# Performance work log

Measured on AMD Instinct MI355X. Metric: run time of the kernel, lower is better.

The kernel has to match this reference:

```python
import jax, jax.numpy as jnp
import numpy as np

B, T, I, H, O = 256, 1024, 128, 256, 64


def setup_inputs() -> dict:
    key = jax.random.key(0)
    ks = jax.random.split(key, 8)
    s_ih = 1.0 / np.sqrt(H)
    return {
        "x": jax.random.normal(ks[0], (B, T, I), dtype=jnp.float32),
        "W_ih": jax.random.normal(ks[1], (3 * H, I), dtype=jnp.float32) * s_ih,
        "W_hh": jax.random.normal(ks[2], (3 * H, H), dtype=jnp.float32) * s_ih,
        "b_ih": jax.random.normal(ks[3], (3 * H,), dtype=jnp.float32) * s_ih,
        "b_hh": jax.random.normal(ks[4], (3 * H,), dtype=jnp.float32) * s_ih,
        "alpha": jax.random.normal(ks[5], (H,), dtype=jnp.float32),
        "fc_w": jax.random.normal(ks[6], (O, H), dtype=jnp.float32) * s_ih,
        "fc_b": jax.random.normal(ks[7], (O,), dtype=jnp.float32) * s_ih,
    }


def _pagru_last_hidden(x, W_ih, W_hh, b_ih, b_hh, alpha):
    # Precompute all input-side gate projections in one big GEMM: [T, B, 3H]
    xg = jnp.einsum("bti,gi->tbg", x, W_ih) + b_ih
    a = jax.nn.sigmoid(alpha)  # per-unit adaptive interpolation gate

    def step(h, gi):
        gh = h @ W_hh.T + b_hh                      # [B, 3H]
        i_r, i_z, i_n = jnp.split(gi, 3, axis=-1)
        h_r, h_z, h_n = jnp.split(gh, 3, axis=-1)
        r = jax.nn.sigmoid(i_r + h_r)
        z = jax.nn.sigmoid(i_z + h_z)
        n = jnp.tanh(i_n + r * h_n)
        h_new = (1.0 - z) * n + z * h               # torch GRUCell convention
        h_out = a * h_new + (1.0 - a) * h           # parameter-adaptive update
        return h_out, None

    h0 = jnp.zeros((x.shape[0], W_hh.shape[1]), dtype=x.dtype)
    h_last, _ = jax.lax.scan(step, h0, xg)
    return h_last


def reference(x, W_ih, W_hh, b_ih, b_hh, alpha, fc_w, fc_b):
    h_last = _pagru_last_hidden(x, W_ih, W_hh, b_ih, b_hh, alpha)
    return jax.nn.sigmoid(h_last @ fc_w.T + fc_b)   # [B, O]
```

## Files before the change

kernel.cpp:

```cpp
#include <hip/hip_runtime.h>
#include <cstdint>
#include <cstddef>

#define TT 1024
#define BB 256
#define II 128
#define HH 256
#define GG 768
#define OO 64
#define TCH 256
#define NCH (TT / TCH)

typedef float f32x4 __attribute__((ext_vector_type(4)));
typedef short short8 __attribute__((ext_vector_type(8)));

__device__ __forceinline__ unsigned f2bf(float f) {
  unsigned u = __builtin_bit_cast(unsigned, f);
  return (u + 0x7FFFu + ((u >> 16) & 1u)) >> 16;
}
__device__ __forceinline__ float bflo(unsigned p) {
  return __builtin_bit_cast(float, p << 16);
}
__device__ __forceinline__ float bfhi(unsigned p) {
  return __builtin_bit_cast(float, p & 0xffff0000u);
}
__device__ __forceinline__ unsigned cvtpk_bf16(float lo, float hi) {
  unsigned r;
  asm("v_cvt_pk_bf16_f32 %0, %1, %2" : "=v"(r) : "v"(lo), "v"(hi));
  return r;
}
__device__ __forceinline__ float sigm(float x) {
  return __builtin_amdgcn_rcpf(1.f + __builtin_amdgcn_exp2f(-1.44269504088896f * x));
}

__global__ void k_btot(const float* __restrict__ bih, const float* __restrict__ bhh,
                       float* __restrict__ btot) {
  int i = blockIdx.x * 256 + threadIdx.x;
  if (i < GG) btot[i] = bih[i] + (i < 512 ? bhh[i] : 0.f);
}

__global__ __attribute__((amdgpu_flat_work_group_size(512, 512), amdgpu_waves_per_eu(2, 2)))
void k_xg(const float* __restrict__ x,
    const float* __restrict__ Wih, const float* __restrict__ btot,
    unsigned short* __restrict__ xg, int t0)
{
  __shared__ unsigned short xlds[BB * II];
  const int tid = threadIdx.x;
  const int tl = blockIdx.x;
  const int tg = t0 + tl;
  const int w = tid >> 6, lane = tid & 63, cu = lane & 15, quad = lane >> 4;

  for (int i = 0; i < 16; ++i) {
    int cid = tid + i * 512;
    int row = cid >> 5, c16 = cid & 31;
    const float4 v = *(const float4*)(x + (size_t)row * TT * II + (size_t)tg * II + c16 * 4);
    unsigned lo = f2bf(v.x) | (f2bf(v.y) << 16);
    unsigned hi = f2bf(v.z) | (f2bf(v.w) << 16);
    int byt = (row * 256 + c16 * 8) ^ ((row & 7) << 4);
    *(uint2*)((char*)xlds + byt) = make_uint2(lo, hi);
  }

  uint4 WA[3][2][4];
  float bias[3][2][4];
  #pragma unroll
  for (int pp = 0; pp < 3; ++pp)
    #pragma unroll
    for (int t2 = 0; t2 < 2; ++t2) {
      int ut = w * 6 + pp * 2 + t2;
      int grow = ut * 16 + cu;
      const float4* wr = (const float4*)(Wih + (size_t)grow * II);
      #pragma unroll
      for (int kk = 0; kk < 4; ++kk) {
        float4 lo = wr[kk * 8 + quad * 2];
        float4 hi = wr[kk * 8 + quad * 2 + 1];
        uint4 pk;
        pk.x = f2bf(lo.x) | (f2bf(lo.y) << 16);
        pk.y = f2bf(lo.z) | (f2bf(lo.w) << 16);
        pk.z = f2bf(hi.x) | (f2bf(hi.y) << 16);
        pk.w = f2bf(hi.z) | (f2bf(hi.w) << 16);
        WA[pp][t2][kk] = pk;
      }
      #pragma unroll
      for (int j = 0; j < 4; ++j)
        bias[pp][t2][j] = btot[ut * 16 + quad * 4 + j];
    }
  __syncthreads();

  #pragma unroll 1
  for (int mt = 0; mt < 16; ++mt) {
    short8 bf[4];
    int brow = mt * 16 + cu;
    #pragma unroll
    for (int kk = 0; kk < 4; ++kk) {
      int byt = (brow * 256 + kk * 64 + quad * 16) ^ ((cu & 7) << 4);
      bf[kk] = *(const short8*)((const char*)xlds + byt);
    }
    f32x4 acc[3][2];
    #pragma unroll
    for (int pp = 0; pp < 3; ++pp) {
      acc[pp][0] = (f32x4){0.f, 0.f, 0.f, 0.f};
      acc[pp][1] = (f32x4){0.f, 0.f, 0.f, 0.f};
    }
    #pragma unroll
    for (int kk = 0; kk < 4; ++kk)
      #pragma unroll
      for (int pp = 0; pp < 3; ++pp)
        #pragma unroll
        for (int t2 = 0; t2 < 2; ++t2)
          acc[pp][t2] = __builtin_amdgcn_mfma_f32_16x16x32_bf16(
              __builtin_bit_cast(short8, WA[pp][t2][kk]), bf[kk], acc[pp][t2], 0, 0, 0);
    #pragma unroll
    for (int pp = 0; pp < 3; ++pp)
      #pragma unroll
      for (int t2 = 0; t2 < 2; ++t2) {
        int ut = w * 6 + pp * 2 + t2;
        unsigned p0 = cvtpk_bf16(acc[pp][t2][0] + bias[pp][t2][0],
                                 acc[pp][t2][1] + bias[pp][t2][1]);
        unsigned p1 = cvtpk_bf16(acc[pp][t2][2] + bias[pp][t2][2],
                                 acc[pp][t2][3] + bias[pp][t2][3]);
        size_t rec = ((size_t)(tl * 16 + mt) * 48 + ut) * 64 + lane;
        ((uint2*)xg)[rec] = make_uint2(p0, p1);
      }
  }
}

__global__ __launch_bounds__(1024, 4) void k_scan(const float* __restrict__ Whh,
    const float* __restrict__ bhh, const float* __restrict__ alpha,
    const unsigned short* __restrict__ xg, float* __restrict__ hlast, int t0)
{
  __shared__ unsigned short hbuf[2][16384];
  __shared__ uint4 wlds[16][3][64];
  const int tid = threadIdx.x, wv = tid >> 6, lane = tid & 63;
  const int cu = lane & 15, quad = lane >> 4;
  const int wg = blockIdx.x;

  uint4 Wf[3][7];
  #pragma unroll
  for (int g = 0; g < 3; ++g) {
    int grow = g * 256 + wv * 16 + cu;
    const float4* wr = (const float4*)(Whh + (size_t)grow * HH);
    #pragma unroll
    for (int kk = 0; kk < 8; ++kk) {
      float4 lo = wr[kk * 8 + quad * 2];
      float4 hi = wr[kk * 8 + quad * 2 + 1];
      uint4 pk;
      pk.x = cvtpk_bf16(lo.x, lo.y);
      pk.y = cvtpk_bf16(lo.z, lo.w);
      pk.z = cvtpk_bf16(hi.x, hi.y);
      pk.w = cvtpk_bf16(hi.z, hi.w);
      if (kk < 7) Wf[g][kk] = pk;
      else        wlds[wv][g][lane] = pk;
    }
  }
  const int u0 = wv * 16 + quad * 4;
  unsigned asigp[2], bhp[2];
  asigp[0] = cvtpk_bf16(sigm(alpha[u0]),     sigm(alpha[u0 + 1]));
  asigp[1] = cvtpk_bf16(sigm(alpha[u0 + 2]), sigm(alpha[u0 + 3]));
  bhp[0] = f2bf(bhh[512 + u0])     | (f2bf(bhh[512 + u0 + 1]) << 16);
  bhp[1] = f2bf(bhh[512 + u0 + 2]) | (f2bf(bhh[512 + u0 + 3]) << 16);

  for (int i = 0; i < 4; ++i) {
    int idx = tid * 4 + i;
    int m = idx >> 8, u = idx & 255;
    float hv = (t0 == 0) ? 0.f : hlast[((size_t)wg * 16 + m) * 256 + u];
    int byt = (m * 512 + u * 2) ^ ((m & 7) << 4) ^ ((m >> 3) << 6);
    *(unsigned short*)((char*)hbuf[0] + byt) = (unsigned short)f2bf(hv);
  }
  __syncthreads();

  const unsigned swz = (unsigned)(((cu & 7) << 4) ^ ((cu >> 3) << 6));
  const unsigned vb  = (unsigned)((cu * 512 + quad * 16)) ^ swz;
  const unsigned whp = (unsigned)((cu * 512 + wv * 32 + quad * 8)) ^ swz;

  const uint2* xq = (const uint2*)xg + ((size_t)wg * 48 + wv) * 64 + lane;
  uint2 qn0 = xq[0], qn1 = xq[1024], qn2 = xq[2048];

  unsigned bufb = 0;
  const char* hbase = (const char*)hbuf;

  for (int tl = 0; tl < TCH; ++tl) {
    const char* hs = hbase + bufb;
    f32x4 acc[3];
    acc[0][0]=bflo(qn0.x); acc[0][1]=bfhi(qn0.x); acc[0][2]=bflo(qn0.y); acc[0][3]=bfhi(qn0.y);
    acc[1][0]=bflo(qn1.x); acc[1][1]=bfhi(qn1.x); acc[1][2]=bflo(qn1.y); acc[1][3]=bfhi(qn1.y);
    acc[2][0]=bflo(bhp[0]); acc[2][1]=bfhi(bhp[0]);
    acc[2][2]=bflo(bhp[1]); acc[2][3]=bfhi(bhp[1]);
    uint2 q2c = qn2;
    if (tl < TCH - 1) xq += 49152;
    qn0 = xq[0]; qn1 = xq[1024]; qn2 = xq[2048];
    uint2 hpq = *(const uint2*)(hs + whp);

    #pragma unroll
    for (int kk = 0; kk < 7; ++kk) {
      short8 bfh = *(const short8*)(hs + (vb ^ (unsigned)(kk * 64)));
      #pragma unroll
      for (int g = 0; g < 3; ++g)
        acc[g] = __builtin_amdgcn_mfma_f32_16x16x32_bf16(
            __builtin_bit_cast(short8, Wf[g][kk]), bfh, acc[g], 0, 0, 0);
    }
    {
      short8 bfh = *(const short8*)(hs + (vb ^ (unsigned)(7 * 64)));
      #pragma unroll
      for (int g = 0; g < 3; ++g) {
        short8 wf = __builtin_bit_cast(short8, wlds[wv][g][lane]);
        acc[g] = __builtin_amdgcn_mfma_f32_16x16x32_bf16(wf, bfh, acc[g], 0, 0, 0);
      }
    }

    float hpv[4] = {bflo(hpq.x), bfhi(hpq.x), bflo(hpq.y), bfhi(hpq.y)};
    float xgn[4] = {bflo(q2c.x), bfhi(q2c.x), bflo(q2c.y), bfhi(q2c.y)};
    float av[4]  = {bflo(asigp[0]), bfhi(asigp[0]), bflo(asigp[1]), bfhi(asigp[1])};
    float ho[4];
    #pragma unroll
    for (int j = 0; j < 4; ++j) {
      float rr = sigm(acc[0][j]);
      float ss = sigm(-acc[1][j]);
      float v  = fmaf(rr, acc[2][j], xgn[j]);
      float nn = 1.f - 2.f * __builtin_amdgcn_rcpf(
                     1.f + __builtin_amdgcn_exp2f(2.88539008177793f * v));
      ho[j] = fmaf(av[j] * ss, nn - hpv[j], hpv[j]);
    }
    unsigned p0 = cvtpk_bf16(ho[0], ho[1]);
    unsigned p1 = cvtpk_bf16(ho[2], ho[3]);
    *(uint2*)((char*)hbase + (bufb ^ 32768u) + whp) = make_uint2(p0, p1);
    if (tl == TCH - 1) {
      #pragma unroll
      for (int j = 0; j < 4; ++j)
        hlast[((size_t)wg * 16 + cu) * 256 + u0 + j] = ho[j];
    }
    __syncthreads();
    bufb ^= 32768u;
  }
}

__global__ void k_out(const float* __restrict__ hlast, const float* __restrict__ fcw,
                      const float* __restrict__ fcb, float* __restrict__ out)
{
  int g = blockIdx.x * 256 + threadIdx.x;
  int b = g >> 6, o = g & 63;
  const float* hr = hlast + (size_t)b * HH;
  const float* wr = fcw + (size_t)o * HH;
  float acc = fcb[o];
  for (int u = 0; u < HH; ++u) acc = fmaf(hr[u], wr[u], acc);
  out[g] = sigm(acc);
}

extern "C" void kernel_launch(void* const* d_in, const int* in_sizes, int n_in,
                              void* d_out, int out_size, void* d_ws, size_t ws_size,
                              hipStream_t stream)
{
  const float* x   = (const float*)d_in[0];
  const float* Wih = (const float*)d_in[1];
  const float* Whh = (const float*)d_in[2];
  const float* bih = (const float*)d_in[3];
  const float* bhh = (const float*)d_in[4];
  const float* alp = (const float*)d_in[5];
  const float* fcw = (const float*)d_in[6];
  const float* fcb = (const float*)d_in[7];
  float* out = (float*)d_out;

  const size_t XGB   = (size_t)TCH * 16 * 48 * 64 * 8;
  const size_t HLB   = (size_t)BB * HH * 4;
  const size_t BTB   = (size_t)GG * 4;
  if (ws_size < XGB + HLB + BTB) return;

  unsigned short* xg = (unsigned short*)d_ws;
  float* hlast = (float*)((char*)d_ws + XGB);
  float* btot  = (float*)((char*)d_ws + XGB + HLB);

  k_btot<<<3, 256, 0, stream>>>(bih, bhh, btot);
  for (int c = 0; c < NCH; ++c) {
    k_xg  <<<TCH, 512, 0, stream>>>(x, Wih, btot, xg, c * TCH);
    k_scan<<<16, 1024, 0, stream>>>(Whh, bhh, alp, xg, hlast, c * TCH);
  }
  k_out<<<64, 256, 0, stream>>>(hlast, fcw, fcb, out);
}
```

Before: 1.641 ms.

## Fuse next-chunk input projection into scan launch with double-buffered xg

Merges the input-gate GEMM for chunk c+1 into the same launch as the recurrent scan for chunk c. Extra workgroups beyond the 16 scan blocks compute the next chunk's projections into a second ping-pong buffer. This lets the GEMM run on idle CUs while the latency-bound scan proceeds. The chunk size drops from 256 to 64 timesteps, which shrinks the buffers but means four times as many launches, each reloading W_hh and the h state.

```diff
diff --git a/kernel.cpp b/kernel.cpp
--- a/kernel.cpp
+++ b/kernel.cpp
@@ -8,7 +8,7 @@
 #define HH 256
 #define GG 768
 #define OO 64
-#define TCH 256
+#define TCH 64
 #define NCH (TT / TCH)
 
 typedef float f32x4 __attribute__((ext_vector_type(4)));
@@ -124,15 +124,101 @@
   }
 }
 
-__global__ __launch_bounds__(1024, 4) void k_scan(const float* __restrict__ Whh,
+__global__ __launch_bounds__(1024, 4) void k_fused(const float* __restrict__ Whh,
     const float* __restrict__ bhh, const float* __restrict__ alpha,
-    const unsigned short* __restrict__ xg, float* __restrict__ hlast, int t0)
+    const unsigned short* __restrict__ xg_rd, float* __restrict__ hlast, int t0,
+    const float* __restrict__ x, const float* __restrict__ Wih,
+    const float* __restrict__ btot, unsigned short* __restrict__ xg_wr)
 {
   __shared__ unsigned short hbuf[2][16384];
   __shared__ uint4 wlds[16][3][64];
   const int tid = threadIdx.x, wv = tid >> 6, lane = tid & 63;
   const int cu = lane & 15, quad = lane >> 4;
   const int wg = blockIdx.x;
+
+  if (wg >= 16) {
+    unsigned short* xlds = (unsigned short*)hbuf;
+    const int tl = wg - 16;
+    const int tg = t0 + TCH + tl;
+
+    for (int i = 0; i < 8; ++i) {
+      int cid = tid + i * 1024;
+      int row = cid >> 5, c16 = cid & 31;
+      const float4 v = *(const float4*)(x + (size_t)row * TT * II + (size_t)tg * II + c16 * 4);
+      unsigned lo = f2bf(v.x) | (f2bf(v.y) << 16);
+      unsigned hi = f2bf(v.z) | (f2bf(v.w) << 16);
+      int byt = (row * 256 + c16 * 8) ^ ((row & 7) << 4);
+      *(uint2*)((char*)xlds + byt) = make_uint2(lo, hi);
+    }
+
+    uint4 WA[3][2][4];
+    float bias[3][2][4];
+    const int w = tid >> 6;
+    if (tid < 512) {
+      #pragma unroll
+      for (int pp = 0; pp < 3; ++pp)
+        #pragma unroll
+        for (int t2 = 0; t2 < 2; ++t2) {
+          int ut = w * 6 + pp * 2 + t2;
+          int grow = ut * 16 + cu;
+          const float4* wr = (const float4*)(Wih + (size_t)grow * II);
+          #pragma unroll
+          for (int kk = 0; kk < 4; ++kk) {
+            float4 lo = wr[kk * 8 + quad * 2];
+            float4 hi = wr[kk * 8 + quad * 2 + 1];
+            uint4 pk;
+            pk.x = f2bf(lo.x) | (f2bf(lo.y) << 16);
+            pk.y = f2bf(lo.z) | (f2bf(lo.w) << 16);
+            pk.z = f2bf(hi.x) | (f2bf(hi.y) << 16);
+            pk.w = f2bf(hi.z) | (f2bf(hi.w) << 16);
+            WA[pp][t2][kk] = pk;
+          }
+          #pragma unroll
+          for (int j = 0; j < 4; ++j)
+            bias[pp][t2][j] = btot[ut * 16 + quad * 4 + j];
+        }
+    }
+    __syncthreads();
+    if (tid >= 512) return;
+
+    #pragma unroll 1
+    for (int mt = 0; mt < 16; ++mt) {
+      short8 bf[4];
+      int brow = mt * 16 + cu;
+      #pragma unroll
+      for (int kk = 0; kk < 4; ++kk) {
+        int byt = (brow * 256 + kk * 64 + quad * 16) ^ ((cu & 7) << 4);
+        bf[kk] = *(const short8*)((const char*)xlds + byt);
+      }
+      f32x4 acc[3][2];
+      #pragma unroll
+      for (int pp = 0; pp < 3; ++pp) {
+        acc[pp][0] = (f32x4){0.f, 0.f, 0.f, 0.f};
+        acc[pp][1] = (f32x4){0.f, 0.f, 0.f, 0.f};
+      }
+      #pragma unroll
+      for (int kk = 0; kk < 4; ++kk)
+        #pragma unroll
+        for (int pp = 0; pp < 3; ++pp)
+          #pragma unroll
+          for (int t2 = 0; t2 < 2; ++t2)
+            acc[pp][t2] = __builtin_amdgcn_mfma_f32_16x16x32_bf16(
+                __builtin_bit_cast(short8, WA[pp][t2][kk]), bf[kk], acc[pp][t2], 0, 0, 0);
+      #pragma unroll
+      for (int pp = 0; pp < 3; ++pp)
+        #pragma unroll
+        for (int t2 = 0; t2 < 2; ++t2) {
+          int ut = w * 6 + pp * 2 + t2;
+          unsigned p0 = cvtpk_bf16(acc[pp][t2][0] + bias[pp][t2][0],
+                                   acc[pp][t2][1] + bias[pp][t2][1]);
+          unsigned p1 = cvtpk_bf16(acc[pp][t2][2] + bias[pp][t2][2],
+                                   acc[pp][t2][3] + bias[pp][t2][3]);
+          size_t rec = ((size_t)(tl * 16 + mt) * 48 + ut) * 64 + lane;
+          ((uint2*)xg_wr)[rec] = make_uint2(p0, p1);
+        }
+    }
+    return;
+  }
 
   uint4 Wf[3][7];
   #pragma unroll
@@ -172,7 +258,7 @@
   const unsigned vb  = (unsigned)((cu * 512 + quad * 16)) ^ swz;
   const unsigned whp = (unsigned)((cu * 512 + wv * 32 + quad * 8)) ^ swz;
 
-  const uint2* xq = (const uint2*)xg + ((size_t)wg * 48 + wv) * 64 + lane;
+  const uint2* xq = (const uint2*)xg_rd + ((size_t)wg * 48 + wv) * 64 + lane;
   uint2 qn0 = xq[0], qn1 = xq[1024], qn2 = xq[2048];
 
   unsigned bufb = 0;
@@ -259,19 +345,24 @@
   const float* fcb = (const float*)d_in[7];
   float* out = (float*)d_out;
 
-  const size_t XGB   = (size_t)TCH * 16 * 48 * 64 * 8;
-  const size_t HLB   = (size_t)BB * HH * 4;
-  const size_t BTB   = (size_t)GG * 4;
-  if (ws_size < XGB + HLB + BTB) return;
-
-  unsigned short* xg = (unsigned short*)d_ws;
-  float* hlast = (float*)((char*)d_ws + XGB);
-  float* btot  = (float*)((char*)d_ws + XGB + HLB);
+  const size_t XGB1 = (size_t)TCH * 16 * 48 * 64 * 8;
+  const size_t HLB  = (size_t)BB * HH * 4;
+  const size_t BTB  = (size_t)GG * 4;
+  if (ws_size < 2 * XGB1 + HLB + BTB) return;
+
+  unsigned short* xgA = (unsigned short*)d_ws;
+  unsigned short* xgB = (unsigned short*)((char*)d_ws + XGB1);
+  float* hlast = (float*)((char*)d_ws + 2 * XGB1);
+  float* btot  = (float*)((char*)d_ws + 2 * XGB1 + HLB);
 
   k_btot<<<3, 256, 0, stream>>>(bih, bhh, btot);
+  k_xg<<<TCH, 512, 0, stream>>>(x, Wih, btot, xgA, 0);
   for (int c = 0; c < NCH; ++c) {
-    k_xg  <<<TCH, 512, 0, stream>>>(x, Wih, btot, xg, c * TCH);
-    k_scan<<<16, 1024, 0, stream>>>(Whh, bhh, alp, xg, hlast, c * TCH);
+    unsigned short* rd = (c & 1) ? xgB : xgA;
+    unsigned short* wr = (c & 1) ? xgA : xgB;
+    int nxg = (c + 1 < NCH) ? TCH : 0;
+    k_fused<<<16 + nxg, 1024, 0, stream>>>(Whh, bhh, alp, rd, hlast, c * TCH,
+                                           x, Wih, btot, wr);
   }
   k_out<<<64, 256, 0, stream>>>(hlast, fcw, fcb, out);
 }
```

After: 1.825 ms. 11.2% more time.
